# Performance work log

Measured on AMD Instinct MI355X. Metric: run time of the kernel, lower is better.

Reference implementation:

```python
import jax, jax.numpy as jnp
import numpy as np

EPS = 1e-16


def setup_inputs() -> dict:
    key = jax.random.key(0)
    k1, k2, k3 = jax.random.split(key, 3)
    nnz, d = 2_000_000, 64
    num_cols = 50_000
    values = jax.random.normal(k1, (nnz, d), dtype=jnp.float32)
    rows = jax.random.randint(k2, (nnz,), 0, num_cols, dtype=jnp.int64)
    cols = jax.random.randint(k3, (nnz,), 0, num_cols, dtype=jnp.int64)
    indices = jnp.stack([rows, cols], axis=0)  # [2, nnz]
    return {"values": values, "indices": indices, "num_cols": num_cols}


def reference(values, indices, num_cols):
    # axis=0: pool over rows -> one pooled vector per column (segment mean),
    # then gather-broadcast back to every nonzero entry.
    seg = indices[1]  # index[1 - axis], the column index of each nnz entry
    # segment sum of values: dense [num_cols, d]
    sums = jax.ops.segment_sum(values, seg, num_segments=num_cols)
    # count of nnz per column (+ eps, matching the torch code)
    cnt = jax.ops.segment_sum(
        jnp.ones(values.shape[0], dtype=values.dtype), seg, num_segments=num_cols
    ) + EPS
    mean = sums / cnt[:, None]  # [num_cols, d]
    return mean[seg]  # [nnz, d]
```

## Files before the change

### kernel.cpp

```cpp
#include <hip/hip_runtime.h>

#define EPS 1e-16f
#define STRIDE 96

typedef float f32x4 __attribute__((ext_vector_type(4)));


__global__ void zero_cnt_kernel(int* __restrict__ ws, const int* __restrict__ nc_p) {
    const int nc = *nc_p;
    for (int i = blockIdx.x * blockDim.x + threadIdx.x; i < nc;
         i += gridDim.x * blockDim.x)
        ws[i] = 0;
}

__global__ void append_kernel(const int* __restrict__ cols, int* __restrict__ ws,
                              const int* __restrict__ nc_p, int nnz) {
    const int nc = *nc_p;
    int* cnt  = ws;
    int* perm = ws + nc;
    const int i = blockIdx.x * blockDim.x + threadIdx.x;
    if (i < nnz) {
        const int c = cols[i];
        const int r = atomicAdd(&cnt[c], 1);
        if (r < STRIDE) perm[c * STRIDE + r] = i;
    }
}

__global__ void pool_kernel(const f32x4* __restrict__ vals4,
                            int* __restrict__ ws,
                            const int* __restrict__ nc_p,
                            f32x4* __restrict__ out4) {
    const int nc = *nc_p;
    const int* cnt  = ws;
    const int* perm = ws + nc;
    const int lane = threadIdx.x & 63;
    const int g  = lane >> 4;
    const int jv = lane & 15;
    const int wave = blockIdx.x * (blockDim.x >> 6) + (threadIdx.x >> 6);
    const int nw = gridDim.x * (blockDim.x >> 6);
    for (int c = wave; c < nc; c += nw) {
        int n = cnt[c];
        if (n == 0) continue;
        n = (n > STRIDE) ? STRIDE : n;
        const int s = c * STRIDE;
        const int e = s + n;
        f32x4 acc = (f32x4)(0.f);

        int k = s + g;
        for (; k + 12 < e; k += 16) {
            const int i0 = perm[k];
            const int i1 = perm[k + 4];
            const int i2 = perm[k + 8];
            const int i3 = perm[k + 12];
            const f32x4 v0 = __builtin_nontemporal_load(&vals4[(size_t)i0 * 16 + jv]);
            const f32x4 v1 = __builtin_nontemporal_load(&vals4[(size_t)i1 * 16 + jv]);
            const f32x4 v2 = __builtin_nontemporal_load(&vals4[(size_t)i2 * 16 + jv]);
            const f32x4 v3 = __builtin_nontemporal_load(&vals4[(size_t)i3 * 16 + jv]);
            acc += (v0 + v1) + (v2 + v3);
        }
        for (; k < e; k += 4) {
            const int i = perm[k];
            acc += __builtin_nontemporal_load(&vals4[(size_t)i * 16 + jv]);
        }

        #pragma unroll
        for (int off = 16; off < 64; off <<= 1) {
            acc.x += __shfl_xor(acc.x, off);
            acc.y += __shfl_xor(acc.y, off);
            acc.z += __shfl_xor(acc.z, off);
            acc.w += __shfl_xor(acc.w, off);
        }
        const float inv = 1.0f / ((float)n + EPS);
        const f32x4 mean = acc * inv;

        k = s + g;
        for (; k + 12 < e; k += 16) {
            const int i0 = perm[k];
            const int i1 = perm[k + 4];
            const int i2 = perm[k + 8];
            const int i3 = perm[k + 12];
            __builtin_nontemporal_store(mean, &out4[(size_t)i0 * 16 + jv]);
            __builtin_nontemporal_store(mean, &out4[(size_t)i1 * 16 + jv]);
            __builtin_nontemporal_store(mean, &out4[(size_t)i2 * 16 + jv]);
            __builtin_nontemporal_store(mean, &out4[(size_t)i3 * 16 + jv]);
        }
        for (; k < e; k += 4) {
            const int i = perm[k];
            __builtin_nontemporal_store(mean, &out4[(size_t)i * 16 + jv]);
        }
    }
}

extern "C" void kernel_launch(void* const* d_in, const int* in_sizes, int n_in,
                              void* d_out, int out_size, void* d_ws, size_t ws_size,
                              hipStream_t stream) {
    const float* values  = (const float*)d_in[0];
    const int*   indices = (const int*)d_in[1];
    const int*   nc_p    = (const int*)d_in[2];

    const int nnz = in_sizes[0] / 64;
    const int* cols = indices + nnz;

    int* ws = (int*)d_ws;

    const int blk = 256;
    const int grid_nnz = (nnz + blk - 1) / blk;

    zero_cnt_kernel<<<64, blk, 0, stream>>>(ws, nc_p);
    append_kernel<<<grid_nnz, blk, 0, stream>>>(cols, ws, nc_p, nnz);
    pool_kernel<<<4096, blk, 0, stream>>>((const f32x4*)values, ws, nc_p,
                                          (f32x4*)d_out);
}
```

Measured before the change: 391.3 us.

## Split pooling into per-column mean table plus coalesced gather-broadcast kernel

The pooling kernel now writes each column's mean once into its bucket region of the workspace, overwriting the already-consumed permutation slots. A new gather kernel then streams over the output in linear order, looking up each entry's column and copying the mean from that compact table. Output stores become sequential and coalesced instead of scattered through the permutation, and the mean table is small enough to likely stay cache-resident. The cost is an extra kernel launch and a second read of the column indices.

```diff
diff --git a/kernel.cpp b/kernel.cpp
--- a/kernel.cpp
+++ b/kernel.cpp
@@ -26,13 +26,12 @@
     }
 }
 
-__global__ void pool_kernel(const f32x4* __restrict__ vals4,
-                            int* __restrict__ ws,
-                            const int* __restrict__ nc_p,
-                            f32x4* __restrict__ out4) {
+__global__ void pool_sum_kernel(const f32x4* __restrict__ vals4,
+                                int* __restrict__ ws,
+                                const int* __restrict__ nc_p) {
     const int nc = *nc_p;
     const int* cnt  = ws;
-    const int* perm = ws + nc;
+    int* perm = ws + nc;
     const int lane = threadIdx.x & 63;
     const int g  = lane >> 4;
     const int jv = lane & 15;
@@ -73,21 +72,26 @@
         const float inv = 1.0f / ((float)n + EPS);
         const f32x4 mean = acc * inv;
 
-        k = s + g;
-        for (; k + 12 < e; k += 16) {
-            const int i0 = perm[k];
-            const int i1 = perm[k + 4];
-            const int i2 = perm[k + 8];
-            const int i3 = perm[k + 12];
-            __builtin_nontemporal_store(mean, &out4[(size_t)i0 * 16 + jv]);
-            __builtin_nontemporal_store(mean, &out4[(size_t)i1 * 16 + jv]);
-            __builtin_nontemporal_store(mean, &out4[(size_t)i2 * 16 + jv]);
-            __builtin_nontemporal_store(mean, &out4[(size_t)i3 * 16 + jv]);
+        if (g == 0) {
+            f32x4* bucket4 = (f32x4*)(perm + s);
+            bucket4[jv] = mean;
         }
-        for (; k < e; k += 4) {
-            const int i = perm[k];
-            __builtin_nontemporal_store(mean, &out4[(size_t)i * 16 + jv]);
-        }
+    }
+}
+
+__global__ void gather_kernel(const int* __restrict__ cols,
+                              const int* __restrict__ ws,
+                              const int* __restrict__ nc_p,
+                              f32x4* __restrict__ out4, int nnz) {
+    const int nc = *nc_p;
+    const f32x4* table = (const f32x4*)(ws + nc);
+    const long total = (long)nnz * 16;
+    for (long t = blockIdx.x * (long)blockDim.x + threadIdx.x; t < total;
+         t += (long)gridDim.x * blockDim.x) {
+        const int i  = (int)(t >> 4);
+        const int jv = (int)(t & 15);
+        const int c  = cols[i];
+        __builtin_nontemporal_store(table[(size_t)c * 24 + jv], &out4[t]);
     }
 }
 
@@ -108,6 +112,6 @@
 
     zero_cnt_kernel<<<64, blk, 0, stream>>>(ws, nc_p);
     append_kernel<<<grid_nnz, blk, 0, stream>>>(cols, ws, nc_p, nnz);
-    pool_kernel<<<4096, blk, 0, stream>>>((const f32x4*)values, ws, nc_p,
-                                          (f32x4*)d_out);
+    pool_sum_kernel<<<4096, blk, 0, stream>>>((const f32x4*)values, ws, nc_p);
+    gather_kernel<<<4096, blk, 0, stream>>>(cols, ws, nc_p, (f32x4*)d_out, nnz);
 }
```

New measurement: 458.0 us. +17.0%, slower.
